# Kernel tuning notes

Hardware: AMD Instinct MI355X
Metric: run time of the kernel (lower is better)

The kernel has to match this reference:

```python
import jax, jax.numpy as jnp
import numpy as np
from jax import lax

NEG = jnp.float32(-1e9)
POS = jnp.float32(1e9)


def _edt_sq(mask):
    """Exact squared Euclidean distance transform of a 2D boolean mask.

    mask: [H, W] bool, True = foreground (nonzero in scipy terms).
    Returns [H, W] float32 squared distance to nearest background (False) pixel.
    Felzenszwalb-Huttenlocher separable formulation:
      pass 1 (axis 0): 1D distance to nearest zero per column (O(H) via scans)
      pass 2 (axis 1): min-plus convolution with quadratic per row.
    """
    H, W = mask.shape
    zero = ~mask
    idx = jnp.broadcast_to(jnp.arange(H, dtype=jnp.float32)[:, None], (H, W))
    # index of last background pixel at-or-above, and next at-or-below, per column
    last0 = lax.associative_scan(jnp.maximum, jnp.where(zero, idx, NEG), axis=0)
    next0 = jnp.flip(
        lax.associative_scan(jnp.minimum, jnp.flip(jnp.where(zero, idx, POS), 0), axis=0), 0)
    d1 = jnp.minimum(idx - last0, next0 - idx)  # 1D distance along axis 0
    f = jnp.where(mask, d1 * d1, jnp.float32(0.0))  # squared axis-0 distance
    # pass 2: D[i, j] = min_j' f[i, j'] + (j - j')^2
    jq = jnp.arange(W, dtype=jnp.float32)
    q = (jq[:, None] - jq[None, :]) ** 2  # [W, W]
    def row_min(frow):  # frow: [W]
        return jnp.min(frow[None, :] + q, axis=1)  # [W]
    return lax.map(row_min, f)  # [H, W]


def setup_inputs() -> dict:
    key = jax.random.key(0)
    img = jax.random.uniform(key, (2048, 2048), dtype=jnp.float32)
    return {"img": img}


def reference(img) -> jnp.ndarray:
    mask = img > 0.5  # scipy: nonzero pixels are foreground
    d = jnp.sqrt(_edt_sq(mask))
    m = jnp.max(d)
    d = jnp.where(m > 0, d / m * 255.0, d)  # `if img.max() != 0: img = img/max*255`
    return d.astype(jnp.uint8)  # img.astype(np.uint8)
```

## Files before the change

### kernel.cpp

```cpp
#include <hip/hip_runtime.h>
#include <math.h>

typedef unsigned long long u64;

#define H 2048
#define W 2048
#define NWR 64
#define TILE 128
#define HALOC 16
#define LW 160
#define LSTRIDE 161
#define DCLAMP 2900
#define NTHR 256
#define NBLK 1024

#define TAG_V  0x33C0FFEEull
#define TAG_F  0x44C0FFEEull

__device__ __attribute__((noinline)) int vfar_up_img(const float* img, int col, int r, int rtop) {
    for (int rr = rtop - 1; rr >= 0; --rr)
        if (img[(size_t)rr * W + col] <= 0.5f) return r - rr;
    return DCLAMP;
}
__device__ __attribute__((noinline)) int vfar_dn_img(const float* img, int col, int r, int rbot) {
    for (int rr = rbot + 1; rr < H; ++rr)
        if (img[(size_t)rr * W + col] <= 0.5f) return rr - r;
    return DCLAMP;
}
__device__ __attribute__((noinline)) float f_from_img(const float* img, int col, int r) {
    if (img[(size_t)r * W + col] <= 0.5f) return 0.0f;
    int du = DCLAMP, dn = DCLAMP;
    for (int dd = 1; r - dd >= 0; ++dd)
        if (img[(size_t)(r - dd) * W + col] <= 0.5f) { du = dd; break; }
    for (int dd = 1; r + dd < H; ++dd)
        if (img[(size_t)(r + dd) * W + col] <= 0.5f) { dn = dd; break; }
    int d1 = min(min(du, dn), DCLAMP);
    return (float)d1 * (float)d1;
}

__global__ void __launch_bounds__(NTHR, 4)
edt_solo(const float* __restrict__ img, int* __restrict__ out,
         u64* __restrict__ vcell, u64* __restrict__ flag) {
    __shared__ float ftile[32][LSTRIDE];
    __shared__ float smax[5];
    const int tid = threadIdx.x;
    const int c0 = blockIdx.x * TILE;
    const int ks = blockIdx.y;
    const int rbase = ks * 32;
    const int bid = ks * (W / TILE) + blockIdx.x;

    if (tid < LW) {
        int gc = c0 - HALOC + tid;
        if (gc >= 0 && gc < W) {
            u64 Wv = 0;
            if (ks > 0) {
#pragma unroll
                for (int i = 0; i < 16; ++i)
                    Wv |= (u64)(img[(size_t)(rbase - 16 + i) * W + gc] <= 0.5f) << i;
            }
#pragma unroll
            for (int i = 16; i < 48; ++i)
                Wv |= (u64)(img[(size_t)(rbase - 16 + i) * W + gc] <= 0.5f) << i;
            if (ks < NWR - 1) {
#pragma unroll
                for (int i = 48; i < 64; ++i)
                    Wv |= (u64)(img[(size_t)(rbase - 16 + i) * W + gc] <= 0.5f) << i;
            }
#pragma unroll
            for (int i = 0; i < 32; ++i) {
                const int p = 16 + i;
                u64 lo = Wv & ((1ull << p) - 1ull);
                int da = lo ? (p - (63 - __clzll(lo)))
                            : vfar_up_img(img, gc, rbase + i, rbase - 16);
                u64 hi = Wv >> (p + 1);
                int db = hi ? __ffsll(hi)
                            : vfar_dn_img(img, gc, rbase + i, rbase + 47);
                int d1 = min(min(da, db), DCLAMP);
                float fd = (float)d1;
                ftile[i][tid] = ((Wv >> p) & 1ull) ? 0.0f : fd * fd;
            }
        } else {
#pragma unroll
            for (int i = 0; i < 32; ++i)
                ftile[i][tid] = 1e9f;
        }
    }
    __syncthreads();

    const int i  = tid & 31;
    const int p  = tid >> 5;
    const int lc = HALOC + p * 16;
    float reg[32];
#pragma unroll
    for (int k = 0; k < 32; ++k)
        reg[k] = ftile[i][lc - 8 + k];

    float res[16];
    float lmax = 0.0f;
#pragma unroll
    for (int m = 0; m < 16; ++m) {
        float best = reg[m + 8];
#pragma unroll
        for (int d = 1; d <= 8; ++d) {
            float q = (float)(d * d);
            best = fminf(best, reg[m + 8 - d] + q);
            best = fminf(best, reg[m + 8 + d] + q);
        }
        if (__builtin_expect(81.0f < best, 0)) {
            for (int d = 9; d <= HALOC && (float)(d * d) < best; ++d) {
                float q = (float)(d * d);
                best = fminf(best, ftile[i][lc + m - d] + q);
                best = fminf(best, ftile[i][lc + m + d] + q);
            }
            if ((float)((HALOC + 1) * (HALOC + 1)) < best) {
                int r = rbase + i, jj = c0 + p * 16 + m;
                for (int d = HALOC + 1; d < W && (float)(d * d) < best; ++d) {
                    float q = (float)(d * d);
                    int jm = jj - d, jp = jj + d;
                    if (jm >= 0) best = fminf(best, f_from_img(img, jm, r) + q);
                    if (jp < W)  best = fminf(best, f_from_img(img, jp, r) + q);
                }
            }
        }
        float rr = sqrtf(best);
        res[m] = rr;
        lmax = fmaxf(lmax, rr);
    }

    __syncthreads();
#pragma unroll
    for (int m = 0; m < 16; ++m)
        ftile[i][p * 16 + m] = res[m];

    for (int o = 32; o > 0; o >>= 1) lmax = fmaxf(lmax, __shfl_down(lmax, o, 64));
    if ((tid & 63) == 0) smax[1 + (tid >> 6)] = lmax;
    __syncthreads();

    if (tid == 0) {
        float bm = fmaxf(fmaxf(smax[1], smax[2]), fmaxf(smax[3], smax[4]));
        u64 v = (TAG_V << 32) | (u64)__float_as_uint(bm);
        __hip_atomic_store(&vcell[bid], v, __ATOMIC_RELAXED, __HIP_MEMORY_SCOPE_AGENT);
    }
    if (bid == 0) {
        u64 v[NBLK / NTHR];
        bool ready;
        do {
            ready = true;
#pragma unroll
            for (int k = 0; k < NBLK / NTHR; ++k)
                v[k] = __hip_atomic_load(&vcell[tid * (NBLK / NTHR) + k],
                                         __ATOMIC_RELAXED, __HIP_MEMORY_SCOPE_AGENT);
#pragma unroll
            for (int k = 0; k < NBLK / NTHR; ++k)
                ready &= ((v[k] >> 32) == TAG_V);
            if (!ready) __builtin_amdgcn_s_sleep(2);
        } while (!ready);
        float mv = 0.0f;
#pragma unroll
        for (int k = 0; k < NBLK / NTHR; ++k)
            mv = fmaxf(mv, __uint_as_float((unsigned)v[k]));
        for (int o = 32; o > 0; o >>= 1) mv = fmaxf(mv, __shfl_down(mv, o, 64));
        if ((tid & 63) == 0) smax[1 + (tid >> 6)] = mv;
        __syncthreads();
        if (tid == 0) {
            float gm = fmaxf(fmaxf(smax[1], smax[2]), fmaxf(smax[3], smax[4]));
            smax[0] = gm;
            u64 v2 = (TAG_F << 32) | (u64)__float_as_uint(gm);
            __hip_atomic_store(flag, v2, __ATOMIC_RELAXED, __HIP_MEMORY_SCOPE_AGENT);
        }
    } else if (tid == 0) {
        u64 v;
        while (((v = __hip_atomic_load(flag, __ATOMIC_RELAXED,
                                       __HIP_MEMORY_SCOPE_AGENT)) >> 32) != TAG_F)
            __builtin_amdgcn_s_sleep(8);
        smax[0] = __uint_as_float((unsigned)v);
    }
    __syncthreads();

    float m = smax[0];
    float scale = (m > 0.0f) ? 1.0f / m : 0.0f;
#pragma unroll
    for (int q = 0; q < 4; ++q) {
        int r  = (tid >> 5) + 8 * q;
        int c4 = (tid & 31) * 4;
        int o[4];
#pragma unroll
        for (int k = 0; k < 4; ++k) {
            float dv = ftile[r][c4 + k];
            float v = (m > 0.0f) ? (dv * scale * 255.0f) : dv;
            v = fminf(fmaxf(v, 0.0f), 255.0f);
            o[k] = (int)v;
        }
        *(int4*)(out + (size_t)(rbase + r) * W + c0 + c4) = make_int4(o[0], o[1], o[2], o[3]);
    }
}

extern "C" void kernel_launch(void* const* d_in, const int* in_sizes, int n_in,
                              void* d_out, int out_size, void* d_ws, size_t ws_size,
                              hipStream_t stream) {
    const float* img = (const float*)d_in[0];
    int* out = (int*)d_out;

    u64* vcell = (u64*)d_ws;
    u64* flag  = (u64*)((char*)d_ws + 8192 + 128);

    edt_solo<<<dim3(W / TILE, NWR), dim3(NTHR), 0, stream>>>(img, out, vcell, flag);
}
```

Measured before the change: 80.68 us.

## Shrink column halo, branchless vertical distance with deferred fixups, prefetch results

The column halo drops from 16 to 8, so the shared tile is narrower, and the in-tile extended search beyond radius 8 now goes straight to the global-image fallback. The vertical distance computation becomes branchless, using sentinel bits, and records rare out-of-window cases in a bitmask that is fixed up afterwards. This avoids per-row divergent calls. Final tile values are read into registers before the grid-wide max wait, and the spin-wait sleep is shortened. The risk is that pixels needing a horizontal search past radius 8 now do slow global scans.

```diff
diff --git a/kernel.cpp b/kernel.cpp
--- a/kernel.cpp
+++ b/kernel.cpp
@@ -7,9 +7,9 @@
 #define W 2048
 #define NWR 64
 #define TILE 128
-#define HALOC 16
-#define LW 160
-#define LSTRIDE 161
+#define HALOC 8
+#define LW 144
+#define LSTRIDE 145
 #define DCLAMP 2900
 #define NTHR 256
 #define NBLK 1024
@@ -66,18 +66,36 @@
                 for (int i = 48; i < 64; ++i)
                     Wv |= (u64)(img[(size_t)(rbase - 16 + i) * W + gc] <= 0.5f) << i;
             }
+            unsigned fixmask = 0;
 #pragma unroll
             for (int i = 0; i < 32; ++i) {
                 const int p = 16 + i;
                 u64 lo = Wv & ((1ull << p) - 1ull);
-                int da = lo ? (p - (63 - __clzll(lo)))
-                            : vfar_up_img(img, gc, rbase + i, rbase - 16);
                 u64 hi = Wv >> (p + 1);
-                int db = hi ? __ffsll(hi)
-                            : vfar_dn_img(img, gc, rbase + i, rbase + 47);
+                int da = p - (63 - __clzll(lo | 1ull));
+                int db = __ffsll(hi | 0x8000000000000000ull);
+                fixmask |= ((lo == 0) | (hi == 0)) ? (1u << i) : 0u;
                 int d1 = min(min(da, db), DCLAMP);
                 float fd = (float)d1;
                 ftile[i][tid] = ((Wv >> p) & 1ull) ? 0.0f : fd * fd;
+            }
+            if (__builtin_expect(fixmask != 0, 0)) {
+                do {
+                    int i = __ffs(fixmask) - 1;
+                    fixmask &= fixmask - 1;
+                    const int p = 16 + i;
+                    if (!((Wv >> p) & 1ull)) {
+                        u64 lo = Wv & ((1ull << p) - 1ull);
+                        u64 hi = Wv >> (p + 1);
+                        int da = lo ? (p - (63 - __clzll(lo)))
+                                    : vfar_up_img(img, gc, rbase + i, rbase - 16);
+                        int db = hi ? __ffsll(hi)
+                                    : vfar_dn_img(img, gc, rbase + i, rbase + 47);
+                        int d1 = min(min(da, db), DCLAMP);
+                        float fd = (float)d1;
+                        ftile[i][tid] = fd * fd;
+                    }
+                } while (fixmask);
             }
         } else {
 #pragma unroll
@@ -107,19 +125,12 @@
             best = fminf(best, reg[m + 8 + d] + q);
         }
         if (__builtin_expect(81.0f < best, 0)) {
-            for (int d = 9; d <= HALOC && (float)(d * d) < best; ++d) {
+            int r = rbase + i, jj = c0 + p * 16 + m;
+            for (int d = 9; d < W && (float)(d * d) < best; ++d) {
                 float q = (float)(d * d);
-                best = fminf(best, ftile[i][lc + m - d] + q);
-                best = fminf(best, ftile[i][lc + m + d] + q);
-            }
-            if ((float)((HALOC + 1) * (HALOC + 1)) < best) {
-                int r = rbase + i, jj = c0 + p * 16 + m;
-                for (int d = HALOC + 1; d < W && (float)(d * d) < best; ++d) {
-                    float q = (float)(d * d);
-                    int jm = jj - d, jp = jj + d;
-                    if (jm >= 0) best = fminf(best, f_from_img(img, jm, r) + q);
-                    if (jp < W)  best = fminf(best, f_from_img(img, jp, r) + q);
-                }
+                int jm = jj - d, jp = jj + d;
+                if (jm >= 0) best = fminf(best, f_from_img(img, jm, r) + q);
+                if (jp < W)  best = fminf(best, f_from_img(img, jp, r) + q);
             }
         }
         float rr = sqrtf(best);
@@ -135,6 +146,16 @@
     for (int o = 32; o > 0; o >>= 1) lmax = fmaxf(lmax, __shfl_down(lmax, o, 64));
     if ((tid & 63) == 0) smax[1 + (tid >> 6)] = lmax;
     __syncthreads();
+
+    float pre[16];
+#pragma unroll
+    for (int q = 0; q < 4; ++q) {
+        int r  = (tid >> 5) + 8 * q;
+        int c4 = (tid & 31) * 4;
+#pragma unroll
+        for (int k = 0; k < 4; ++k)
+            pre[q * 4 + k] = ftile[r][c4 + k];
+    }
 
     if (tid == 0) {
         float bm = fmaxf(fmaxf(smax[1], smax[2]), fmaxf(smax[3], smax[4]));
@@ -172,7 +193,7 @@
         u64 v;
         while (((v = __hip_atomic_load(flag, __ATOMIC_RELAXED,
                                        __HIP_MEMORY_SCOPE_AGENT)) >> 32) != TAG_F)
-            __builtin_amdgcn_s_sleep(8);
+            __builtin_amdgcn_s_sleep(4);
         smax[0] = __uint_as_float((unsigned)v);
     }
     __syncthreads();
@@ -186,7 +207,7 @@
         int o[4];
 #pragma unroll
         for (int k = 0; k < 4; ++k) {
-            float dv = ftile[r][c4 + k];
+            float dv = pre[q * 4 + k];
             float v = (m > 0.0f) ? (dv * scale * 255.0f) : dv;
             v = fminf(fmaxf(v, 0.0f), 255.0f);
             o[k] = (int)v;
```

Result: no change. 82.27 us (+2.0%).
